# Kernel tuning notes

Hardware: AMD Instinct MI355X
Metric: run time of the kernel (lower is better)

The kernel has to match this reference:

```python
import jax, jax.numpy as jnp
import numpy as np

B, L, D = 16, 512, 512
T_MAX = 4096  # mel_max_length: static pad target (upper bound on sum of durations)


def setup_inputs() -> dict:
    key = jax.random.key(0)
    kx, kd = jax.random.split(key)
    x = jax.random.normal(kx, (B, L, D), dtype=jnp.float32)
    duration_tokens = jax.random.randint(kd, (B, L), 0, 8, dtype=jnp.int32)
    return {"x": x, "duration_tokens": duration_tokens, "mel_max_length": T_MAX}


def reference(x, duration_tokens, mel_max_length):
    # LengthRegulator: out[b, t] = x[b, j] where token j covers output frame t,
    # i.e. the alignment matmul  alignment @ x  expressed as cumsum + searchsorted + gather.
    b, l, d = x.shape
    ends = jnp.cumsum(duration_tokens, axis=1)            # [B, L] exclusive frame ends
    t = jnp.arange(mel_max_length, dtype=ends.dtype)      # [T]
    # token index covering each frame t: first j with ends[j] > t
    tok = jax.vmap(lambda e: jnp.searchsorted(e, t, side='right'))(ends)  # [B, T]
    valid = t[None, :] < ends[:, -1:]                     # frames beyond total duration -> zero pad
    tok = jnp.clip(tok, 0, l - 1)
    out = jnp.take_along_axis(x, tok[:, :, None], axis=1)  # [B, T, D]
    return jnp.where(valid[:, :, None], out, jnp.zeros((), dtype=x.dtype))
```

## Files before the change

### kernel.cpp

```cpp
#include <hip/hip_runtime.h>


#define BATCH 16
#define LTOK  512
#define DIM   512
#define TMAX  4096
#define ROWS  8

typedef float nt_f4 __attribute__((ext_vector_type(4)));

__global__ __launch_bounds__(512) void MRTE_cumsum_kernel(const int* __restrict__ dur,
                                                          int* __restrict__ ends) {
    const int b    = blockIdx.x;
    const int tid  = threadIdx.x;
    const int lane = tid & 63;
    const int wid  = tid >> 6;
    __shared__ int wsum[8];

    int v = dur[b * LTOK + tid];
    #pragma unroll
    for (int off = 1; off < 64; off <<= 1) {
        int n = __shfl_up(v, off, 64);
        if (lane >= off) v += n;
    }
    if (lane == 63) wsum[wid] = v;
    __syncthreads();
    int add = 0;
    #pragma unroll
    for (int w = 0; w < 7; ++w)
        add += (w < wid) ? wsum[w] : 0;
    ends[b * LTOK + tid] = v + add;
}

__global__ __launch_bounds__(256) void MRTE_gather_kernel(const float* __restrict__ x,
                                                          const int* __restrict__ ends,
                                                          float* __restrict__ out) {
    __shared__ int se[LTOK];
    const int b    = blockIdx.y;
    const int t0   = blockIdx.x * ROWS;
    const int tid  = threadIdx.x;
    const int half = tid >> 7;
    const int lane = tid & 127;

    se[tid]       = ends[b * LTOK + tid];
    se[tid + 256] = ends[b * LTOK + tid + 256];
    __syncthreads();

    const int total = se[LTOK - 1];

    int lo = 0, hi = LTOK;
    while (lo < hi) {
        int mid = (lo + hi) >> 1;
        if (se[mid] > t0) hi = mid; else lo = mid + 1;
    }

    const nt_f4* __restrict__ xb =
        reinterpret_cast<const nt_f4*>(x + (size_t)b * LTOK * DIM);
    nt_f4* __restrict__ ob =
        reinterpret_cast<nt_f4*>(out + ((size_t)b * TMAX + (size_t)t0) * DIM);

    int jt = lo;
    #pragma unroll
    for (int r = 0; r < ROWS; r += 2) {
        const int t = t0 + r + half;
        nt_f4 v = (nt_f4)0.f;
        if (t < total) {
            while (se[jt] <= t) ++jt;
            v = xb[(size_t)jt * (DIM / 4) + lane];
        }
        __builtin_nontemporal_store(v, &ob[(size_t)(r + half) * (DIM / 4) + lane]);
    }
}

extern "C" void kernel_launch(void* const* d_in, const int* in_sizes, int n_in,
                              void* d_out, int out_size, void* d_ws, size_t ws_size,
                              hipStream_t stream) {
    const float* x   = (const float*)d_in[0];
    const int*   dur = (const int*)d_in[1];
    float* out  = (float*)d_out;
    int*   ends = (int*)d_ws;

    MRTE_cumsum_kernel<<<BATCH, LTOK, 0, stream>>>(dur, ends);
    MRTE_gather_kernel<<<dim3(TMAX / ROWS, BATCH), 256, 0, stream>>>(x, ends, out);
}
```

Measured before the change: 159.3 us.

## Fuse duration cumsum into gather kernel, recomputing prefix sums per block

Removes the separate cumsum kernel and its workspace round trip. Each gather block now loads the 512 durations with one wavefront, does a per-thread serial scan of 8 values and a wave shuffle scan, and writes the ends into shared memory. This drops one kernel launch and the dependency between two kernels. In exchange, every block repeats a small scan and the other waves sit idle at the barrier while it runs.

```diff
diff --git a/kernel.cpp b/kernel.cpp
--- a/kernel.cpp
+++ b/kernel.cpp
@@ -9,32 +9,9 @@
 
 typedef float nt_f4 __attribute__((ext_vector_type(4)));
 
-__global__ __launch_bounds__(512) void MRTE_cumsum_kernel(const int* __restrict__ dur,
-                                                          int* __restrict__ ends) {
-    const int b    = blockIdx.x;
-    const int tid  = threadIdx.x;
-    const int lane = tid & 63;
-    const int wid  = tid >> 6;
-    __shared__ int wsum[8];
-
-    int v = dur[b * LTOK + tid];
-    #pragma unroll
-    for (int off = 1; off < 64; off <<= 1) {
-        int n = __shfl_up(v, off, 64);
-        if (lane >= off) v += n;
-    }
-    if (lane == 63) wsum[wid] = v;
-    __syncthreads();
-    int add = 0;
-    #pragma unroll
-    for (int w = 0; w < 7; ++w)
-        add += (w < wid) ? wsum[w] : 0;
-    ends[b * LTOK + tid] = v + add;
-}
-
-__global__ __launch_bounds__(256) void MRTE_gather_kernel(const float* __restrict__ x,
-                                                          const int* __restrict__ ends,
-                                                          float* __restrict__ out) {
+__global__ __launch_bounds__(256) void MRTE_fused_kernel(const float* __restrict__ x,
+                                                         const int* __restrict__ dur,
+                                                         float* __restrict__ out) {
     __shared__ int se[LTOK];
     const int b    = blockIdx.y;
     const int t0   = blockIdx.x * ROWS;
@@ -42,8 +19,29 @@
     const int half = tid >> 7;
     const int lane = tid & 127;
 
-    se[tid]       = ends[b * LTOK + tid];
-    se[tid + 256] = ends[b * LTOK + tid + 256];
+    if (tid < 64) {
+        const int4* __restrict__ d4 = reinterpret_cast<const int4*>(dur + b * LTOK);
+        int4 a = d4[tid * 2];
+        int4 c = d4[tid * 2 + 1];
+        int p0 = a.x;
+        int p1 = p0 + a.y;
+        int p2 = p1 + a.z;
+        int p3 = p2 + a.w;
+        int p4 = p3 + c.x;
+        int p5 = p4 + c.y;
+        int p6 = p5 + c.z;
+        int p7 = p6 + c.w;
+        int s = p7;
+        #pragma unroll
+        for (int off = 1; off < 64; off <<= 1) {
+            int n = __shfl_up(s, off, 64);
+            if (tid >= off) s += n;
+        }
+        const int base = s - p7;
+        int4* o = reinterpret_cast<int4*>(se + tid * 8);
+        o[0] = make_int4(base + p0, base + p1, base + p2, base + p3);
+        o[1] = make_int4(base + p4, base + p5, base + p6, base + p7);
+    }
     __syncthreads();
 
     const int total = se[LTOK - 1];
@@ -77,9 +75,7 @@
                               hipStream_t stream) {
     const float* x   = (const float*)d_in[0];
     const int*   dur = (const int*)d_in[1];
-    float* out  = (float*)d_out;
-    int*   ends = (int*)d_ws;
+    float* out = (float*)d_out;
 
-    MRTE_cumsum_kernel<<<BATCH, LTOK, 0, stream>>>(dur, ends);
-    MRTE_gather_kernel<<<dim3(TMAX / ROWS, BATCH), 256, 0, stream>>>(x, ends, out);
+    MRTE_fused_kernel<<<dim3(TMAX / ROWS, BATCH), 256, 0, stream>>>(x, dur, out);
 }
```

New measurement: 156.4 us. Within noise of the previous version (-1.8%).
